# Optimization experiments

Measured on AMD Instinct MI355X. Metric: run time of the kernel, lower is better.

## Reference

```python
import jax, jax.numpy as jnp
import numpy as np

B, NQ, NK, D_IN, HD = 1, 16384, 7933, 1024, 512
R = 0.3  # keep-top-r fraction used for the quantile threshold


def _l2norm(x):
    # matches F.normalize(p=2, dim=-1, eps=1e-12)
    n = jnp.linalg.norm(x, axis=-1, keepdims=True)
    return x / jnp.maximum(n, 1e-12)


def setup_inputs() -> dict:
    key = jax.random.key(0)
    ks = jax.random.split(key, 10)
    s = 0.02
    return {
        "query": jax.random.normal(ks[0], (B, NQ, D_IN), jnp.float32),
        "key_x": jax.random.normal(ks[1], (B, NK, D_IN), jnp.float32),
        "wq_w": jax.random.normal(ks[2], (HD, D_IN), jnp.float32) * s,
        "wq_b": jnp.zeros((HD,), jnp.float32),
        "wk_w": jax.random.normal(ks[3], (HD, D_IN), jnp.float32) * s,
        "wk_b": jnp.zeros((HD,), jnp.float32),
        "wa_w": jax.random.normal(ks[4], (1, NK), jnp.float32) * s,
        "wa_b": jnp.zeros((1,), jnp.float32),
        "cls_w": jax.random.normal(ks[5], (1, HD), jnp.float32) * s,
        "cls_b": jnp.zeros((1,), jnp.float32),
    }


def reference(query, key_x, wq_w, wq_b, wk_w, wk_b, wa_w, wa_b, cls_w, cls_b):
    # WQ / WK: Linear + Tanh
    q = jnp.tanh(jnp.einsum("bnd,hd->bnh", query, wq_w) + wq_b)   # [B,NQ,HD]
    k = jnp.tanh(jnp.einsum("bnd,hd->bnh", key_x, wk_w) + wk_b)   # [B,NK,HD]
    # normalized dot-product scores
    A = jnp.einsum("bqh,bkh->bqk", _l2norm(q), _l2norm(k))        # [B,NQ,NK]
    # WA: Linear(NK -> 1)
    A1 = jnp.einsum("bqk,ok->bqo", A, wa_w) + wa_b                # [B,NQ,1]
    # quantile threshold from batch 0 (torch: sorted ascending, index -int(r*NQ))
    thre = jax.lax.stop_gradient(jnp.sort(A1[0, :, 0])[-int(R * NQ)])
    A1 = jnp.where(A1 > thre, A1, 0.0)                            # F.threshold(., thre, 0)
    attn = jax.nn.softmax(A1, axis=1)                             # softmax over NQ (zeros included)
    attn_t = jnp.transpose(attn, (0, 2, 1))                       # [B,1,NQ]
    z = jnp.matmul(attn_t, q).reshape(-1, HD)                     # [B,HD]
    y_prob = z @ cls_w.T + cls_b                                  # [B,1]
    return (y_prob, attn_t)
```

## Files before the change

### kernel.cpp

```cpp
#include <hip/hip_runtime.h>
#include <math.h>

#define NQ 16384
#define NK 7933
#define DI 1024
#define HD 512
#define RANK_TARGET 11469

typedef __bf16 bf16x8 __attribute__((ext_vector_type(8)));
typedef float  f32x4  __attribute__((ext_vector_type(4)));

#define GLOAD_LDS16(g, l)                                                     \
  __builtin_amdgcn_global_load_lds(                                           \
      (const __attribute__((address_space(1))) void*)(g),                     \
      (__attribute__((address_space(3))) void*)(l), 16, 0, 0)

__device__ __forceinline__ unsigned mapf(float f) {
  unsigned b = __float_as_uint(f);
  return (b & 0x80000000u) ? ~b : (b | 0x80000000u);
}

__device__ __forceinline__ bf16x8 cvt8(float4 a, float4 b) {
  bf16x8 o;
  o[0] = (__bf16)a.x; o[1] = (__bf16)a.y; o[2] = (__bf16)a.z; o[3] = (__bf16)a.w;
  o[4] = (__bf16)b.x; o[5] = (__bf16)b.y; o[6] = (__bf16)b.z; o[7] = (__bf16)b.w;
  return o;
}

__global__ void conv_wk(const float* __restrict__ wq, const float* __restrict__ wk,
                        const float* __restrict__ key,
                        __bf16* __restrict__ wqbf, __bf16* __restrict__ wkbf,
                        __bf16* __restrict__ kbf, unsigned* __restrict__ zero_region) {
  if (blockIdx.x == 0) {
    for (int j = threadIdx.x; j < 1088; j += 256) zero_region[j] = 0u;
  }
  const int NK8 = NK * DI / 8;
  const int W8  = HD * DI / 8;
  const int total = NK8 + 2 * W8;
  int i = blockIdx.x * blockDim.x + threadIdx.x;
  int stride = gridDim.x * blockDim.x;
  for (; i < total; i += stride) {
    const float* s; __bf16* d; int j;
    if (i < NK8)            { s = key; d = kbf;  j = i; }
    else if (i < NK8 + W8)  { s = wq;  d = wqbf; j = i - NK8; }
    else                    { s = wk;  d = wkbf; j = i - NK8 - W8; }
    float4 a = ((const float4*)s)[2 * j];
    float4 b = ((const float4*)s)[2 * j + 1];
    ((bf16x8*)d)[j] = cvt8(a, b);
  }
}

template <bool FUSE_A1>
__device__ __forceinline__ void gemm_core(
    const __bf16* __restrict__ A, const __bf16* __restrict__ B,
    const float* __restrict__ bias, float* __restrict__ C, int M,
    int m0, int n0, __bf16* sA, __bf16* sB,
    const float* __restrict__ v, float* __restrict__ A1dot,
    float* __restrict__ A1ss) {
  constexpr int K = DI;
  constexpr int N = HD;
  const int tid  = threadIdx.x;
  const int lane = tid & 63;
  const int wave = tid >> 6;
  const int wr = wave >> 2;
  const int wc = wave & 3;

  const int srow = lane >> 3;
  const int scol = ((lane & 7) ^ srow) << 3;

  const int lrow = lane & 15;
  const int chi  = lane >> 4;

  int gaA = m0 + wave * 8 + srow; if (gaA > M - 1) gaA = M - 1;
  const __bf16* Ap = A + (size_t)gaA * K + scol;
  const __bf16* Bp0 = B + (size_t)(n0 + (wave * 4 + 0) * 8 + srow) * K + scol;
  const __bf16* Bp1 = B + (size_t)(n0 + (wave * 4 + 1) * 8 + srow) * K + scol;
  const __bf16* Bp2 = B + (size_t)(n0 + (wave * 4 + 2) * 8 + srow) * K + scol;
  const __bf16* Bp3 = B + (size_t)(n0 + (wave * 4 + 3) * 8 + srow) * K + scol;

  f32x4 acc[2][4] = {};

  GLOAD_LDS16(Ap, &sA[wave * 512]);
  GLOAD_LDS16(Bp0, &sB[(wave * 4 + 0) * 512]);
  GLOAD_LDS16(Bp1, &sB[(wave * 4 + 1) * 512]);
  GLOAD_LDS16(Bp2, &sB[(wave * 4 + 2) * 512]);
  GLOAD_LDS16(Bp3, &sB[(wave * 4 + 3) * 512]);
  __syncthreads();

  int buf = 0;
  for (int t = 0; t < 16; ++t) {
    const int kk = t * 64;
    if (t < 15) {
      const int ob = (buf ^ 1);
      GLOAD_LDS16(Ap + kk + 64, &sA[ob * 4096 + wave * 512]);
      GLOAD_LDS16(Bp0 + kk + 64, &sB[ob * 16384 + (wave * 4 + 0) * 512]);
      GLOAD_LDS16(Bp1 + kk + 64, &sB[ob * 16384 + (wave * 4 + 1) * 512]);
      GLOAD_LDS16(Bp2 + kk + 64, &sB[ob * 16384 + (wave * 4 + 2) * 512]);
      GLOAD_LDS16(Bp3 + kk + 64, &sB[ob * 16384 + (wave * 4 + 3) * 512]);
    }
    const __bf16* sAc = sA + buf * 4096;
    const __bf16* sBc = sB + buf * 16384;
#pragma unroll
    for (int ks = 0; ks < 64; ks += 32) {
      const int cc = (ks >> 3) + chi;
      const int sw = ((cc ^ (lrow & 7)) << 3);
      bf16x8 af[2], bfr[4];
      af[0] = *(const bf16x8*)(&sAc[(wr * 32 + lrow) * 64 + sw]);
      af[1] = *(const bf16x8*)(&sAc[(wr * 32 + 16 + lrow) * 64 + sw]);
#pragma unroll
      for (int ni = 0; ni < 4; ++ni)
        bfr[ni] = *(const bf16x8*)(&sBc[(wc * 64 + ni * 16 + lrow) * 64 + sw]);
#pragma unroll
      for (int ni = 0; ni < 4; ++ni) {
        acc[0][ni] = __builtin_amdgcn_mfma_f32_16x16x32_bf16(af[0], bfr[ni], acc[0][ni], 0, 0, 0);
        acc[1][ni] = __builtin_amdgcn_mfma_f32_16x16x32_bf16(af[1], bfr[ni], acc[1][ni], 0, 0, 0);
      }
    }
    if (t < 15) {
      __syncthreads();
      buf ^= 1;
    }
  }

  const int rbase = m0 + wr * 32 + ((lane >> 4) << 2);
  const int cbase = n0 + wc * 64 + (lane & 15);
  float b4[4], v4[4];
#pragma unroll
  for (int ni = 0; ni < 4; ++ni) {
    b4[ni] = bias[cbase + ni * 16];
    if constexpr (FUSE_A1) v4[ni] = v[cbase + ni * 16];
  }
#pragma unroll
  for (int mi = 0; mi < 2; ++mi) {
#pragma unroll
    for (int r = 0; r < 4; ++r) {
      int grow = rbase + mi * 16 + r;
      if (grow < M) {
        float pd = 0.f, pss = 0.f;
#pragma unroll
        for (int ni = 0; ni < 4; ++ni) {
          float val = tanhf(acc[mi][ni][r] + b4[ni]);
          C[(size_t)grow * N + cbase + ni * 16] = val;
          if constexpr (FUSE_A1) { pd += val * v4[ni]; pss += val * val; }
        }
        if constexpr (FUSE_A1) {
#pragma unroll
          for (int off = 1; off < 16; off <<= 1) {
            pd += __shfl_xor(pd, off);
            pss += __shfl_xor(pss, off);
          }
          if ((lane & 15) == 0) {
            atomicAdd(&A1dot[grow], pd);
            atomicAdd(&A1ss[grow], pss);
          }
        }
      }
    }
  }
}

__global__ __launch_bounds__(512, 4)
void gemm_k_conv_q(const __bf16* __restrict__ kbf, const __bf16* __restrict__ wkbf,
                   const float* __restrict__ wk_b, float* __restrict__ ktanh,
                   const float* __restrict__ query, __bf16* __restrict__ qbf) {
  __shared__ __align__(16) __bf16 sA[2 * 64 * 64];
  __shared__ __align__(16) __bf16 sB[2 * 256 * 64];
  const int bid = blockIdx.x;
  if (bid < 248) {
    const int m0 = (bid >> 1) * 64;
    const int n0 = (bid & 1) * 256;
    gemm_core<false>(kbf, wkbf, wk_b, ktanh, NK, m0, n0, sA, sB,
                     nullptr, nullptr, nullptr);
  } else {
    const int total = NQ * DI / 8;
    for (int i = (bid - 248) * 512 + threadIdx.x; i < total; i += 264 * 512) {
      float4 a = ((const float4*)query)[2 * i];
      float4 b = ((const float4*)query)[2 * i + 1];
      ((bf16x8*)qbf)[i] = cvt8(a, b);
    }
  }
}

__global__ __launch_bounds__(512, 4)
void gemm_q(const __bf16* __restrict__ qbf, const __bf16* __restrict__ wqbf,
            const float* __restrict__ wq_b, float* __restrict__ qtanh,
            const float* __restrict__ v, float* __restrict__ A1dot,
            float* __restrict__ A1ss) {
  __shared__ __align__(16) __bf16 sA[2 * 64 * 64];
  __shared__ __align__(16) __bf16 sB[2 * 256 * 64];
  gemm_core<true>(qbf, wqbf, wq_b, qtanh, NQ, blockIdx.x * 64, blockIdx.y * 256,
                  sA, sB, v, A1dot, A1ss);
}

__global__ __launch_bounds__(256)
void reduce_v_zero(const float* __restrict__ kt, const float* __restrict__ wa,
                   float* __restrict__ v, int M, uint2* __restrict__ zr) {
  {
    int g = blockIdx.x * 256 + threadIdx.x;
    uint2 zz; zz.x = 0u; zz.y = 0u;
    if (g < 24576) zr[g] = zz;
  }
  __shared__ float vpart[4][512];
  const int tid = threadIdx.x, lane = tid & 63, wave = tid >> 6;
  const int gw = blockIdx.x * 4 + wave;
  const int tw = gridDim.x * 4;
  float acc[8] = {0, 0, 0, 0, 0, 0, 0, 0};
  for (int r = gw; r < M; r += tw) {
    const float4* p = (const float4*)(kt + (size_t)r * HD + lane * 8);
    float4 x = p[0], y = p[1];
    float ss = x.x * x.x + x.y * x.y + x.z * x.z + x.w * x.w
             + y.x * y.x + y.y * y.y + y.z * y.z + y.w * y.w;
#pragma unroll
    for (int off = 32; off; off >>= 1) ss += __shfl_xor(ss, off);
    float s = wa[r] / fmaxf(sqrtf(ss), 1e-12f);
    acc[0] += s * x.x; acc[1] += s * x.y; acc[2] += s * x.z; acc[3] += s * x.w;
    acc[4] += s * y.x; acc[5] += s * y.y; acc[6] += s * y.z; acc[7] += s * y.w;
  }
#pragma unroll
  for (int j = 0; j < 8; ++j) vpart[wave][lane * 8 + j] = acc[j];
  __syncthreads();
  for (int c = tid; c < 512; c += 256)
    atomicAdd(&v[c], vpart[0][c] + vpart[1][c] + vpart[2][c] + vpart[3][c]);
}

__global__ __launch_bounds__(1024)
void select_kernel(const float* __restrict__ A1dot, const float* __restrict__ A1ss,
                   const float* __restrict__ wa_b, float* __restrict__ A1,
                   unsigned* __restrict__ keyg, float* __restrict__ scf) {
  __shared__ unsigned wred1[16], wred2[16], wred3[16];
  __shared__ unsigned s_res;
  const int t = threadIdx.x, lane = t & 63, wave = t >> 6;
  const float wab = wa_b[0];
  unsigned kloc[16];
#pragma unroll 4
  for (int j = 0; j < 16; ++j) {
    int i = j * 1024 + t;
    float d = A1dot[i], ss = A1ss[i];
    float a1 = d / fmaxf(sqrtf(ss), 1e-12f) + wab;
    A1[i] = a1;
    unsigned k = mapf(a1);
    kloc[j] = k;
    keyg[i] = k;
  }
  if (t == 0) s_res = 0u;
  __syncthreads();

  for (int b = 30; b >= 0; b -= 2) {
    const unsigned res = s_res;
    const unsigned t1 = res | (1u << b);
    const unsigned t2 = res | (2u << b);
    const unsigned t3 = res | (3u << b);
    unsigned c1 = 0, c2 = 0, c3 = 0;
#pragma unroll
    for (int j = 0; j < 16; ++j) {
      unsigned k = kloc[j];
      c1 += (k < t1); c2 += (k < t2); c3 += (k < t3);
    }
#pragma unroll
    for (int off = 32; off; off >>= 1) {
      c1 += __shfl_xor(c1, off);
      c2 += __shfl_xor(c2, off);
      c3 += __shfl_xor(c3, off);
    }
    if (lane == 0) { wred1[wave] = c1; wred2[wave] = c2; wred3[wave] = c3; }
    __syncthreads();
    if (t == 0) {
      unsigned C1 = 0, C2 = 0, C3 = 0;
      for (int w = 0; w < 16; ++w) { C1 += wred1[w]; C2 += wred2[w]; C3 += wred3[w]; }
      unsigned nr = res;
      if (C3 <= RANK_TARGET)      nr = t3;
      else if (C2 <= RANK_TARGET) nr = t2;
      else if (C1 <= RANK_TARGET) nr = t1;
      s_res = nr;
    }
    __syncthreads();
  }
  if (t == 0) {
    unsigned key = s_res;
    unsigned bits = (key & 0x80000000u) ? (key ^ 0x80000000u) : ~key;
    scf[0] = __uint_as_float(bits);
  }
}

__global__ __launch_bounds__(256)
void expz(const float* __restrict__ A1, const float* __restrict__ qt,
          float* __restrict__ scf, float* __restrict__ e_out,
          float* __restrict__ z) {
  __shared__ float vpart[4][512];
  __shared__ float esum[4];
  const int tid = threadIdx.x, lane = tid & 63, wave = tid >> 6;
  const float thre = scf[0];
  const int gw = blockIdx.x * 4 + wave;
  const int tw = gridDim.x * 4;
  float acc[8] = {0, 0, 0, 0, 0, 0, 0, 0};
  float es = 0.f;
  for (int r = gw; r < NQ; r += tw) {
    float x = A1[r]; x = (x > thre) ? x : 0.f;
    float e = expf(x - thre);
    if (lane == 0) e_out[r] = e;
    es += e;
    const float4* p = (const float4*)(qt + (size_t)r * HD + lane * 8);
    float4 u = p[0], w = p[1];
    acc[0] += e * u.x; acc[1] += e * u.y; acc[2] += e * u.z; acc[3] += e * u.w;
    acc[4] += e * w.x; acc[5] += e * w.y; acc[6] += e * w.z; acc[7] += e * w.w;
  }
  if (lane == 0) esum[wave] = es;
#pragma unroll
  for (int j = 0; j < 8; ++j) vpart[wave][lane * 8 + j] = acc[j];
  __syncthreads();
  for (int c = tid; c < 512; c += 256)
    atomicAdd(&z[c], vpart[0][c] + vpart[1][c] + vpart[2][c] + vpart[3][c]);
  if (tid == 0) atomicAdd(&scf[2], esum[0] + esum[1] + esum[2] + esum[3]);
}

__global__ __launch_bounds__(256)
void finalize(float* __restrict__ attn, const float* __restrict__ scf,
              const float* __restrict__ z, const float* __restrict__ cls_w,
              const float* __restrict__ cls_b, float* __restrict__ y) {
  const float invZ = 1.f / scf[2];
  if (blockIdx.x < 64) {
    int i = blockIdx.x * 256 + threadIdx.x;
    attn[i] *= invZ;
  } else if (threadIdx.x < 64) {
    const int lane = threadIdx.x;
    const float4* zp = (const float4*)(z + lane * 8);
    const float4* wp = (const float4*)(cls_w + lane * 8);
    float4 a = zp[0], b = zp[1], c = wp[0], d = wp[1];
    float dot = a.x * c.x + a.y * c.y + a.z * c.z + a.w * c.w
              + b.x * d.x + b.y * d.y + b.z * d.z + b.w * d.w;
#pragma unroll
    for (int off = 32; off; off >>= 1) dot += __shfl_xor(dot, off);
    if (lane == 0) y[0] = dot * invZ + cls_b[0];
  }
}

#define OFF_WQBF 0u
#define OFF_WKBF 1048576u
#define OFF_A1D  1048576u
#define OFF_A1S  1114112u
#define OFF_KEY  1179648u
#define OFF_QBF  2097152u
#define OFF_A1   35651584u
#define OFF_V    35717120u
#define OFF_Z    35719168u
#define OFF_SC   35721216u
#define OFF_KBF  35721472u
#define OFF_KT   51968256u
#define OFF_QT   35721472u

extern "C" void kernel_launch(void* const* d_in, const int* in_sizes, int n_in,
                              void* d_out, int out_size, void* d_ws, size_t ws_size,
                              hipStream_t stream) {
  const float* query = (const float*)d_in[0];
  const float* key_x = (const float*)d_in[1];
  const float* wq_w  = (const float*)d_in[2];
  const float* wq_b  = (const float*)d_in[3];
  const float* wk_w  = (const float*)d_in[4];
  const float* wk_b  = (const float*)d_in[5];
  const float* wa_w  = (const float*)d_in[6];
  const float* wa_b  = (const float*)d_in[7];
  const float* cls_w = (const float*)d_in[8];
  const float* cls_b = (const float*)d_in[9];
  float* out = (float*)d_out;

  char* ws = (char*)d_ws;
  __bf16* wqbf  = (__bf16*)(ws + OFF_WQBF);
  __bf16* wkbf  = (__bf16*)(ws + OFF_WKBF);
  float*  A1dot = (float*)(ws + OFF_A1D);
  float*  A1ss  = (float*)(ws + OFF_A1S);
  unsigned* keyg = (unsigned*)(ws + OFF_KEY);
  __bf16* qbf   = (__bf16*)(ws + OFF_QBF);
  float*  A1    = (float*)(ws + OFF_A1);
  float*  v     = (float*)(ws + OFF_V);
  float*  z     = (float*)(ws + OFF_Z);
  float*  scf   = (float*)(ws + OFF_SC);
  __bf16* kbf   = (__bf16*)(ws + OFF_KBF);
  float*  ktanh = (float*)(ws + OFF_KT);
  float*  qtanh = (float*)(ws + OFF_QT);
  float*  out_attn = out + 1;

  conv_wk<<<2048, 256, 0, stream>>>(wq_w, wk_w, key_x, wqbf, wkbf, kbf,
                                    (unsigned*)v);

  gemm_k_conv_q<<<512, 512, 0, stream>>>(kbf, wkbf, wk_b, ktanh, query, qbf);

  reduce_v_zero<<<256, 256, 0, stream>>>(ktanh, wa_w, v, NK, (uint2*)A1dot);

  gemm_q<<<dim3(256, 2), 512, 0, stream>>>(qbf, wqbf, wq_b, qtanh, v, A1dot, A1ss);

  select_kernel<<<1, 1024, 0, stream>>>(A1dot, A1ss, wa_b, A1, keyg, scf);

  expz<<<256, 256, 0, stream>>>(A1, qtanh, scf, out_attn, z);

  finalize<<<65, 256, 0, stream>>>(out_attn, scf, z, cls_w, cls_b, out);
}
```

Baseline: 256.8 us.

## Fuse K-projection GEMM with row-normalized v reduction, drop ktanh buffer

```diff
diff --git a/kernel.cpp b/kernel.cpp
--- a/kernel.cpp
+++ b/kernel.cpp
@@ -30,9 +30,14 @@
 __global__ void conv_wk(const float* __restrict__ wq, const float* __restrict__ wk,
                         const float* __restrict__ key,
                         __bf16* __restrict__ wqbf, __bf16* __restrict__ wkbf,
-                        __bf16* __restrict__ kbf, unsigned* __restrict__ zero_region) {
+                        __bf16* __restrict__ kbf, unsigned* __restrict__ zero_region,
+                        uint2* __restrict__ a1zero) {
   if (blockIdx.x == 0) {
     for (int j = threadIdx.x; j < 1088; j += 256) zero_region[j] = 0u;
+  } else if (blockIdx.x < 65) {
+    int g = (blockIdx.x - 1) * 256 + threadIdx.x;
+    uint2 zz; zz.x = 0u; zz.y = 0u;
+    a1zero[g] = zz;
   }
   const int NK8 = NK * DI / 8;
   const int W8  = HD * DI / 8;
@@ -67,12 +72,11 @@
 
   const int srow = lane >> 3;
   const int scol = ((lane & 7) ^ srow) << 3;
-
   const int lrow = lane & 15;
   const int chi  = lane >> 4;
 
   int gaA = m0 + wave * 8 + srow; if (gaA > M - 1) gaA = M - 1;
-  const __bf16* Ap = A + (size_t)gaA * K + scol;
+  const __bf16* Ap  = A + (size_t)gaA * K + scol;
   const __bf16* Bp0 = B + (size_t)(n0 + (wave * 4 + 0) * 8 + srow) * K + scol;
   const __bf16* Bp1 = B + (size_t)(n0 + (wave * 4 + 1) * 8 + srow) * K + scol;
   const __bf16* Bp2 = B + (size_t)(n0 + (wave * 4 + 2) * 8 + srow) * K + scol;
@@ -80,7 +84,7 @@
 
   f32x4 acc[2][4] = {};
 
-  GLOAD_LDS16(Ap, &sA[wave * 512]);
+  GLOAD_LDS16(Ap,  &sA[wave * 512]);
   GLOAD_LDS16(Bp0, &sB[(wave * 4 + 0) * 512]);
   GLOAD_LDS16(Bp1, &sB[(wave * 4 + 1) * 512]);
   GLOAD_LDS16(Bp2, &sB[(wave * 4 + 2) * 512]);
@@ -92,7 +96,7 @@
     const int kk = t * 64;
     if (t < 15) {
       const int ob = (buf ^ 1);
-      GLOAD_LDS16(Ap + kk + 64, &sA[ob * 4096 + wave * 512]);
+      GLOAD_LDS16(Ap + kk + 64,  &sA[ob * 4096 + wave * 512]);
       GLOAD_LDS16(Bp0 + kk + 64, &sB[ob * 16384 + (wave * 4 + 0) * 512]);
       GLOAD_LDS16(Bp1 + kk + 64, &sB[ob * 16384 + (wave * 4 + 1) * 512]);
       GLOAD_LDS16(Bp2 + kk + 64, &sB[ob * 16384 + (wave * 4 + 2) * 512]);
@@ -159,25 +163,139 @@
   }
 }
 
-__global__ __launch_bounds__(512, 4)
-void gemm_k_conv_q(const __bf16* __restrict__ kbf, const __bf16* __restrict__ wkbf,
-                   const float* __restrict__ wk_b, float* __restrict__ ktanh,
-                   const float* __restrict__ query, __bf16* __restrict__ qbf) {
+__global__ __launch_bounds__(512, 2)
+void gemm_k_fused(const __bf16* __restrict__ kbf, const __bf16* __restrict__ wkbf,
+                  const float* __restrict__ wk_b, const float* __restrict__ wa,
+                  float* __restrict__ v,
+                  const float* __restrict__ query, __bf16* __restrict__ qbf) {
   __shared__ __align__(16) __bf16 sA[2 * 64 * 64];
-  __shared__ __align__(16) __bf16 sB[2 * 256 * 64];
+  __shared__ __align__(16) __bf16 sB[2 * 512 * 64];
+  __shared__ float ssrow[64];
   const int bid = blockIdx.x;
-  if (bid < 248) {
-    const int m0 = (bid >> 1) * 64;
-    const int n0 = (bid & 1) * 256;
-    gemm_core<false>(kbf, wkbf, wk_b, ktanh, NK, m0, n0, sA, sB,
-                     nullptr, nullptr, nullptr);
-  } else {
+  const int tid = threadIdx.x;
+
+  if (bid >= 124) {
     const int total = NQ * DI / 8;
-    for (int i = (bid - 248) * 512 + threadIdx.x; i < total; i += 264 * 512) {
+    for (int i = (bid - 124) * 512 + tid; i < total; i += 132 * 512) {
       float4 a = ((const float4*)query)[2 * i];
       float4 b = ((const float4*)query)[2 * i + 1];
       ((bf16x8*)qbf)[i] = cvt8(a, b);
     }
+    return;
+  }
+
+  constexpr int K = DI;
+  const int lane = tid & 63;
+  const int wave = tid >> 6;
+  const int m0 = bid * 64;
+
+  const int srow = lane >> 3;
+  const int scol = ((lane & 7) ^ srow) << 3;
+  const int lrow = lane & 15;
+  const int chi  = lane >> 4;
+
+  int gaA = m0 + wave * 8 + srow; if (gaA > NK - 1) gaA = NK - 1;
+  const __bf16* Ap = kbf + (size_t)gaA * K + scol;
+  const __bf16* Bp[8];
+#pragma unroll
+  for (int c = 0; c < 8; ++c)
+    Bp[c] = wkbf + (size_t)(wave * 64 + c * 8 + srow) * K + scol;
+
+  f32x4 acc[4][4] = {};
+
+  GLOAD_LDS16(Ap, &sA[wave * 512]);
+#pragma unroll
+  for (int c = 0; c < 8; ++c)
+    GLOAD_LDS16(Bp[c], &sB[(wave * 8 + c) * 512]);
+  __syncthreads();
+
+  int buf = 0;
+  for (int t = 0; t < 16; ++t) {
+    const int kk = t * 64;
+    if (t < 15) {
+      const int ob = buf ^ 1;
+      GLOAD_LDS16(Ap + kk + 64, &sA[ob * 4096 + wave * 512]);
+#pragma unroll
+      for (int c = 0; c < 8; ++c)
+        GLOAD_LDS16(Bp[c] + kk + 64, &sB[ob * 32768 + (wave * 8 + c) * 512]);
+    }
+    const __bf16* sAc = sA + buf * 4096;
+    const __bf16* sBc = sB + buf * 32768;
+#pragma unroll
+    for (int ks = 0; ks < 64; ks += 32) {
+      const int cc = (ks >> 3) + chi;
+      const int sw = ((cc ^ (lrow & 7)) << 3);
+      bf16x8 af[4], bfr[4];
+#pragma unroll
+      for (int mi = 0; mi < 4; ++mi)
+        af[mi] = *(const bf16x8*)(&sAc[(mi * 16 + lrow) * 64 + sw]);
+#pragma unroll
+      for (int ni = 0; ni < 4; ++ni)
+        bfr[ni] = *(const bf16x8*)(&sBc[(wave * 64 + ni * 16 + lrow) * 64 + sw]);
+#pragma unroll
+      for (int mi = 0; mi < 4; ++mi)
+#pragma unroll
+        for (int ni = 0; ni < 4; ++ni)
+          acc[mi][ni] = __builtin_amdgcn_mfma_f32_16x16x32_bf16(af[mi], bfr[ni], acc[mi][ni], 0, 0, 0);
+    }
+    if (t < 15) { __syncthreads(); buf ^= 1; }
+  }
+
+  if (tid < 64) ssrow[tid] = 0.f;
+  __syncthreads();
+
+  float b4[4];
+#pragma unroll
+  for (int ni = 0; ni < 4; ++ni) b4[ni] = wk_b[wave * 64 + ni * 16 + lrow];
+
+#pragma unroll
+  for (int mi = 0; mi < 4; ++mi)
+#pragma unroll
+    for (int ni = 0; ni < 4; ++ni)
+#pragma unroll
+      for (int r = 0; r < 4; ++r)
+        acc[mi][ni][r] = tanhf(acc[mi][ni][r] + b4[ni]);
+
+#pragma unroll
+  for (int mi = 0; mi < 4; ++mi)
+#pragma unroll
+    for (int r = 0; r < 4; ++r) {
+      float ps = 0.f;
+#pragma unroll
+      for (int ni = 0; ni < 4; ++ni) ps += acc[mi][ni][r] * acc[mi][ni][r];
+#pragma unroll
+      for (int off = 1; off < 16; off <<= 1) ps += __shfl_xor(ps, off);
+      if ((lane & 15) == 0)
+        atomicAdd(&ssrow[mi * 16 + (lane >> 4) * 4 + r], ps);
+    }
+  __syncthreads();
+
+  if (tid < 64) {
+    int grow = m0 + tid;
+    float s = 0.f;
+    if (grow < NK) s = wa[grow] / fmaxf(sqrtf(ssrow[tid]), 1e-12f);
+    ssrow[tid] = s;
+  }
+  __syncthreads();
+
+  float sc[4][4];
+#pragma unroll
+  for (int mi = 0; mi < 4; ++mi)
+#pragma unroll
+    for (int r = 0; r < 4; ++r)
+      sc[mi][r] = ssrow[mi * 16 + (lane >> 4) * 4 + r];
+
+#pragma unroll
+  for (int ni = 0; ni < 4; ++ni) {
+    float cs = 0.f;
+#pragma unroll
+    for (int mi = 0; mi < 4; ++mi)
+#pragma unroll
+      for (int r = 0; r < 4; ++r)
+        cs += acc[mi][ni][r] * sc[mi][r];
+    cs += __shfl_xor(cs, 16);
+    cs += __shfl_xor(cs, 32);
+    if (lane < 16) atomicAdd(&v[wave * 64 + ni * 16 + lane], cs);
   }
 }
 
@@ -192,41 +310,10 @@
                   sA, sB, v, A1dot, A1ss);
 }
 
-__global__ __launch_bounds__(256)
-void reduce_v_zero(const float* __restrict__ kt, const float* __restrict__ wa,
-                   float* __restrict__ v, int M, uint2* __restrict__ zr) {
-  {
-    int g = blockIdx.x * 256 + threadIdx.x;
-    uint2 zz; zz.x = 0u; zz.y = 0u;
-    if (g < 24576) zr[g] = zz;
-  }
-  __shared__ float vpart[4][512];
-  const int tid = threadIdx.x, lane = tid & 63, wave = tid >> 6;
-  const int gw = blockIdx.x * 4 + wave;
-  const int tw = gridDim.x * 4;
-  float acc[8] = {0, 0, 0, 0, 0, 0, 0, 0};
-  for (int r = gw; r < M; r += tw) {
-    const float4* p = (const float4*)(kt + (size_t)r * HD + lane * 8);
-    float4 x = p[0], y = p[1];
-    float ss = x.x * x.x + x.y * x.y + x.z * x.z + x.w * x.w
-             + y.x * y.x + y.y * y.y + y.z * y.z + y.w * y.w;
-#pragma unroll
-    for (int off = 32; off; off >>= 1) ss += __shfl_xor(ss, off);
-    float s = wa[r] / fmaxf(sqrtf(ss), 1e-12f);
-    acc[0] += s * x.x; acc[1] += s * x.y; acc[2] += s * x.z; acc[3] += s * x.w;
-    acc[4] += s * y.x; acc[5] += s * y.y; acc[6] += s * y.z; acc[7] += s * y.w;
-  }
-#pragma unroll
-  for (int j = 0; j < 8; ++j) vpart[wave][lane * 8 + j] = acc[j];
-  __syncthreads();
-  for (int c = tid; c < 512; c += 256)
-    atomicAdd(&v[c], vpart[0][c] + vpart[1][c] + vpart[2][c] + vpart[3][c]);
-}
-
 __global__ __launch_bounds__(1024)
 void select_kernel(const float* __restrict__ A1dot, const float* __restrict__ A1ss,
                    const float* __restrict__ wa_b, float* __restrict__ A1,
-                   unsigned* __restrict__ keyg, float* __restrict__ scf) {
+                   float* __restrict__ scf) {
   __shared__ unsigned wred1[16], wred2[16], wred3[16];
   __shared__ unsigned s_res;
   const int t = threadIdx.x, lane = t & 63, wave = t >> 6;
@@ -238,9 +325,7 @@
     float d = A1dot[i], ss = A1ss[i];
     float a1 = d / fmaxf(sqrtf(ss), 1e-12f) + wab;
     A1[i] = a1;
-    unsigned k = mapf(a1);
-    kloc[j] = k;
-    keyg[i] = k;
+    kloc[j] = mapf(a1);
   }
   if (t == 0) s_res = 0u;
   __syncthreads();
@@ -336,17 +421,15 @@
 
 #define OFF_WQBF 0u
 #define OFF_WKBF 1048576u
-#define OFF_A1D  1048576u
-#define OFF_A1S  1114112u
-#define OFF_KEY  1179648u
 #define OFF_QBF  2097152u
 #define OFF_A1   35651584u
 #define OFF_V    35717120u
 #define OFF_Z    35719168u
 #define OFF_SC   35721216u
 #define OFF_KBF  35721472u
-#define OFF_KT   51968256u
-#define OFF_QT   35721472u
+#define OFF_QT   52428800u
+#define OFF_A1D  88080384u
+#define OFF_A1S  88145920u
 
 extern "C" void kernel_launch(void* const* d_in, const int* in_sizes, int n_in,
                               void* d_out, int out_size, void* d_ws, size_t ws_size,
@@ -366,29 +449,25 @@
   char* ws = (char*)d_ws;
   __bf16* wqbf  = (__bf16*)(ws + OFF_WQBF);
   __bf16* wkbf  = (__bf16*)(ws + OFF_WKBF);
-  float*  A1dot = (float*)(ws + OFF_A1D);
-  float*  A1ss  = (float*)(ws + OFF_A1S);
-  unsigned* keyg = (unsigned*)(ws + OFF_KEY);
   __bf16* qbf   = (__bf16*)(ws + OFF_QBF);
   float*  A1    = (float*)(ws + OFF_A1);
   float*  v     = (float*)(ws + OFF_V);
   float*  z     = (float*)(ws + OFF_Z);
   float*  scf   = (float*)(ws + OFF_SC);
   __bf16* kbf   = (__bf16*)(ws + OFF_KBF);
-  float*  ktanh = (float*)(ws + OFF_KT);
   float*  qtanh = (float*)(ws + OFF_QT);
+  float*  A1dot = (float*)(ws + OFF_A1D);
+  float*  A1ss  = (float*)(ws + OFF_A1S);
   float*  out_attn = out + 1;
 
   conv_wk<<<2048, 256, 0, stream>>>(wq_w, wk_w, key_x, wqbf, wkbf, kbf,
-                                    (unsigned*)v);
-
-  gemm_k_conv_q<<<512, 512, 0, stream>>>(kbf, wkbf, wk_b, ktanh, query, qbf);
-
-  reduce_v_zero<<<256, 256, 0, stream>>>(ktanh, wa_w, v, NK, (uint2*)A1dot);
+                                    (unsigned*)v, (uint2*)A1dot);
+
+  gemm_k_fused<<<256, 512, 0, stream>>>(kbf, wkbf, wk_b, wa_w, v, query, qbf);
 
   gemm_q<<<dim3(256, 2), 512, 0, stream>>>(qbf, wqbf, wq_b, qtanh, v, A1dot, A1ss);
 
-  select_kernel<<<1, 1024, 0, stream>>>(A1dot, A1ss, wa_b, A1, keyg, scf);
+  select_kernel<<<1, 1024, 0, stream>>>(A1dot, A1ss, wa_b, A1, scf);
 
   expz<<<256, 256, 0, stream>>>(A1, qtanh, scf, out_attn, z);
 
```

Measured after the change: 245.5 us. -4.4%, faster.
